# Kernel tuning notes

Hardware: AMD Instinct MI355X
Metric: run time of the kernel (lower is better)

The kernel has to match this reference:

```python
import jax, jax.numpy as jnp
import numpy as np

B, N, DIM = 2, 512, 128
HEADS, DH = 4, 64
INNER = HEADS * DH            # 256
POS_HID = 64
MULT = 4                      # attn_mlp_hidden_mult
K = 16                        # num_neighbors


def setup_inputs() -> dict:
    key = jax.random.key(0)
    ks = jax.random.split(key, 10)
    w = lambda k, shape: jax.random.normal(k, shape, jnp.float32) * 0.02
    return {
        "x": jax.random.normal(ks[0], (B, N, DIM), jnp.float32),
        "pos": jax.random.normal(ks[1], (B, N, 3), jnp.float32),
        "mask": jnp.ones((B, N), dtype=bool),
        "w_qkv": w(ks[2], (DIM, 3 * INNER)),
        "w_out": w(ks[3], (INNER, DIM)),
        "b_out": jnp.zeros((DIM,), jnp.float32),
        "w_pos1": w(ks[4], (3, POS_HID)),
        "b_pos1": jnp.zeros((POS_HID,), jnp.float32),
        "w_pos2": w(ks[5], (POS_HID, INNER)),
        "b_pos2": jnp.zeros((INNER,), jnp.float32),
        # grouped 1x1 convs == per-head linear layers
        "w_attn1": w(ks[6], (HEADS, DH, MULT * DH)),
        "b_attn1": jnp.zeros((HEADS, MULT * DH), jnp.float32),
        "w_attn2": w(ks[7], (HEADS, MULT * DH, DH)),
        "b_attn2": jnp.zeros((HEADS, DH), jnp.float32),
    }


def reference(x, pos, mask, w_qkv, w_out, b_out, w_pos1, b_pos1, w_pos2, b_pos2,
              w_attn1, b_attn1, w_attn2, b_attn2):
    b, n, _ = x.shape
    h, d = HEADS, DH

    qkv = x @ w_qkv                                   # [b, n, 3*inner]
    q, k, v = jnp.split(qkv, 3, axis=-1)
    to_heads = lambda t: t.reshape(b, n, h, d).transpose(0, 2, 1, 3)  # b h n d
    q, k, v = map(to_heads, (q, k, v))

    # dense pairwise relative positions + pos MLP  [b, n, n, inner]
    rel_pos = pos[:, :, None, :] - pos[:, None, :, :]            # [b, n, n, 3]
    rpe = jax.nn.relu(rel_pos @ w_pos1 + b_pos1) @ w_pos2 + b_pos2

    # masked topk over pairwise distance (smallest K)
    rel_dist = jnp.linalg.norm(rel_pos, axis=-1)                 # [b, n, n]
    mask2 = mask[:, :, None] & mask[:, None, :]                  # [b, n, n]
    fmax = jnp.finfo(rel_dist.dtype).max
    rel_dist = jnp.where(mask2, rel_dist, fmax)
    _, idx = jax.lax.top_k(-rel_dist, K)                         # [b, n, K]

    # neighbor gathers (equivalent to torch batched_index_select over j)
    gather_hd = jax.vmap(lambda t, i: t[:, i, :])                # [h,n,d],[n,K] -> [h,n,K,d]
    k_nb = gather_hd(k, idx)                                     # [b, h, n, K, d]
    v_nb = gather_hd(v, idx)
    row = jnp.arange(n)[:, None]
    rpe_nb = jax.vmap(lambda r, i: r[row, i])(rpe, idx)          # [b, n, K, inner]
    rpe_nb = rpe_nb.reshape(b, n, K, h, d).transpose(0, 3, 1, 2, 4)  # [b,h,n,K,d]
    mask_nb = jax.vmap(lambda m, i: m[row, i])(mask2, idx)       # [b, n, K]

    # qk_rel gathered implicitly: (q_i - k_j)[j=idx] == q_i - k_nb
    attn_in = q[:, :, :, None, :] - k_nb + rpe_nb                # [b, h, n, K, d]

    # grouped 1x1 conv MLP == per-head MLP on last dim
    hid = jax.nn.relu(jnp.einsum('bhikd,hde->bhike', attn_in, w_attn1)
                      + b_attn1[None, :, None, None, :])
    sim = (jnp.einsum('bhike,hed->bhikd', hid, w_attn2)
           + b_attn2[None, :, None, None, :])                    # [b, h, n, K, d]

    sim = jnp.where(mask_nb[:, None, :, :, None], sim, -fmax)
    # torch: sim is [b, (h d), i, j]; softmax(dim=-2) is over i -> axis 2 here
    attn = jax.nn.softmax(sim, axis=2)

    v_full = v_nb + rpe_nb                                       # [b, h, n, K, d]
    agg = jnp.sum(attn * v_full, axis=3)                         # [b, h, n, d]
    agg = agg.transpose(0, 2, 1, 3).reshape(b, n, h * d)         # [b, n, inner]
    return agg @ w_out + b_out
```

## Files before the change

kernel.cpp:

```cpp
#include <hip/hip_runtime.h>

#define B_ 2
#define N_ 512
#define DIM_ 128
#define HEADS_ 4
#define DH_ 64
#define INNER_ 256
#define PH_ 64
#define HID2_ 256
#define KNB_ 16

typedef unsigned long long u64;
typedef unsigned int u32;
typedef unsigned short u16;
typedef __attribute__((ext_vector_type(8))) short bf16x8;
typedef __attribute__((ext_vector_type(8))) unsigned short us8;
typedef __attribute__((ext_vector_type(4))) float f32x4;

__device__ __forceinline__ float bf2f(u16 u) {
    union { float f; u32 u; } c; c.u = ((u32)u) << 16; return c.f;
}
__device__ __forceinline__ u16 f2bf(float f) {
    union { float f; u32 u; } c; c.f = f;
    u32 u = c.u;
    return (u16)((u + 0x7fffu + ((u >> 16) & 1u)) >> 16);
}
__device__ __forceinline__ u32 pack2(float lo, float hi) {
    return ((u32)f2bf(hi) << 16) | (u32)f2bf(lo);
}

__global__ __launch_bounds__(256) void k_front(
        const float* __restrict__ x, const float* __restrict__ pos, const float* __restrict__ w_qkv,
        const float* __restrict__ w_a1, const float* __restrict__ w_a2, const float* __restrict__ w_p2,
        u16* __restrict__ w1T, u16* __restrict__ w2T, u16* __restrict__ w2pT,
        u16* __restrict__ qb, u16* __restrict__ kb, float* __restrict__ v,
        int* __restrict__ idx) {
    int blk = blockIdx.x;
    if (blk < 576) {
        int t = blk * 256 + threadIdx.x;
        if (t < 65536) {
            int h = t >> 14, e = (t >> 6) & 255, d = t & 63;
            w1T[t] = f2bf(w_a1[((h * 64 + d) << 8) + e]);
        } else if (t < 131072) {
            int t2 = t - 65536; int h = t2 >> 14, c = (t2 >> 8) & 63, e = t2 & 255;
            w2T[t2] = f2bf(w_a2[(((h << 8) + e) << 6) + c]);
        } else {
            int t3 = t - 131072; int c = t3 >> 6, e = t3 & 63;
            w2pT[t3] = f2bf(w_p2[(e << 8) + c]);
        }
    } else if (blk < 704) {
        int bu = blk - 576;
        int b = bu >> 6;
        int n0 = (bu & 63) * 8;
        int t = threadIdx.x;
        __shared__ float xs[8][128];
        #pragma unroll
        for (int p = 0; p < 4; ++p) {
            int e = p * 256 + t;
            xs[e >> 7][e & 127] = x[((size_t)(b * N_ + n0) + (e >> 7)) * DIM_ + (e & 127)];
        }
        __syncthreads();
        float acc[3][8];
        #pragma unroll
        for (int cc = 0; cc < 3; ++cc)
            #pragma unroll
            for (int r = 0; r < 8; ++r) acc[cc][r] = 0.f;
        for (int c4 = 0; c4 < 32; ++c4) {
            float wv[3][4];
            #pragma unroll
            for (int dd = 0; dd < 4; ++dd)
                #pragma unroll
                for (int cc = 0; cc < 3; ++cc)
                    wv[cc][dd] = w_qkv[(size_t)(c4 * 4 + dd) * (3 * INNER_) + cc * INNER_ + t];
            #pragma unroll
            for (int r = 0; r < 8; ++r) {
                float4 xv = *(const float4*)&xs[r][c4 * 4];
                #pragma unroll
                for (int cc = 0; cc < 3; ++cc)
                    acc[cc][r] += xv.x * wv[cc][0] + xv.y * wv[cc][1] + xv.z * wv[cc][2] + xv.w * wv[cc][3];
            }
        }
        int h = t >> 6, d = t & 63;
        #pragma unroll
        for (int r = 0; r < 8; ++r) {
            size_t o = (((size_t)(b * HEADS_ + h)) * N_ + n0 + r) * DH_ + d;
            qb[o] = f2bf(acc[0][r]);
            kb[o] = f2bf(acc[1][r]);
            v[o]  = acc[2][r];
        }
    } else {
        int wave = (blk - 704) * 4 + (threadIdx.x >> 6);
        int lane = threadIdx.x & 63;
        int b = wave >> 9;
        float px = pos[(size_t)wave * 3 + 0];
        float py = pos[(size_t)wave * 3 + 1];
        float pz = pos[(size_t)wave * 3 + 2];
        u64 keys[8];
        #pragma unroll
        for (int s = 0; s < 8; ++s) {
            int j = s * 64 + lane;
            float dx = __fsub_rn(px, pos[(size_t)(b * N_ + j) * 3 + 0]);
            float dy = __fsub_rn(py, pos[(size_t)(b * N_ + j) * 3 + 1]);
            float dz = __fsub_rn(pz, pos[(size_t)(b * N_ + j) * 3 + 2]);
            float s2 = __fadd_rn(__fadd_rn(__fmul_rn(dx, dx), __fmul_rn(dy, dy)), __fmul_rn(dz, dz));
            float dist = __fsqrt_rn(s2);
            keys[s] = ((u64)__float_as_uint(dist) << 32) | (unsigned)j;
        }
        for (int r = 0; r < KNB_; ++r) {
            u64 m = keys[0];
            #pragma unroll
            for (int s = 1; s < 8; ++s) m = (keys[s] < m) ? keys[s] : m;
            #pragma unroll
            for (int off = 32; off >= 1; off >>= 1) {
                u64 o = __shfl_xor(m, off);
                m = (o < m) ? o : m;
            }
            if (lane == 0) idx[(size_t)wave * KNB_ + r] = (int)(m & 0xffffffffu);
            #pragma unroll
            for (int s = 0; s < 8; ++s) if (keys[s] == m) keys[s] = ~0ull;
        }
    }
}

__global__ __launch_bounds__(256) void k_attn(
        const u16* __restrict__ qb, const u16* __restrict__ kb, const float* __restrict__ v,
        const int* __restrict__ idx,
        const float* __restrict__ pos, const float* __restrict__ w_p1, const float* __restrict__ b_p1,
        const float* __restrict__ b_p2, const u16* __restrict__ w2pT,
        const u16* __restrict__ w1T, const u16* __restrict__ w2T,
        const float* __restrict__ b_a1, const float* __restrict__ b_a2,
        u16* __restrict__ sim, u16* __restrict__ vf) {
    __shared__ u16 w1s[256 * 72];
    __shared__ u16 w2s[64 * 264];
    __shared__ u16 HID[4][4][16 * 136];
    int t = threadIdx.x;
    int wv = t >> 6, l = t & 63, lr = l & 15, g = l >> 4;
    int blk = blockIdx.x;
    int bh = blk >> 5, grp = blk & 31;
    int b = bh >> 2, h = bh & 3;
    int i0 = grp * 16 + wv * 4;

    int jn[4]; float rx[4], ry[4], rz[4];
    #pragma unroll
    for (int ii = 0; ii < 4; ++ii) {
        int i = i0 + ii, bi = (b << 9) + i;
        int j = idx[(bi << 4) + lr];
        jn[ii] = j;
        int bj = (b << 9) + j;
        rx[ii] = pos[(size_t)bi * 3 + 0] - pos[(size_t)bj * 3 + 0];
        ry[ii] = pos[(size_t)bi * 3 + 1] - pos[(size_t)bj * 3 + 1];
        rz[ii] = pos[(size_t)bi * 3 + 2] - pos[(size_t)bj * 3 + 2];
    }

    {
        const u16* wg = w1T + ((size_t)h << 14);
        #pragma unroll
        for (int p = 0; p < 8; ++p) {
            int c = p * 256 + t;
            int r = c >> 3, c8 = (c & 7) << 3;
            *(bf16x8*)&w1s[r * 72 + c8] = *(const bf16x8*)&wg[(r << 6) + c8];
        }
    }
    {
        const u16* wg = w2T + ((size_t)h << 14);
        #pragma unroll
        for (int p = 0; p < 8; ++p) {
            int c = p * 256 + t;
            int r = c >> 5, c8 = (c & 31) << 3;
            *(bf16x8*)&w2s[r * 264 + c8] = *(const bf16x8*)&wg[(r << 8) + c8];
        }
    }

    bf16x8 hidp[4][2];
    #pragma unroll
    for (int ii = 0; ii < 4; ++ii) {
        #pragma unroll
        for (int s = 0; s < 2; ++s) {
            u16 tmp[8];
            #pragma unroll
            for (int jj = 0; jj < 8; ++jj) {
                int e = s * 32 + g * 8 + jj;
                float hh = b_p1[e] + rx[ii] * w_p1[e] + ry[ii] * w_p1[PH_ + e] + rz[ii] * w_p1[2 * PH_ + e];
                tmp[jj] = f2bf(fmaxf(hh, 0.f));
            }
            hidp[ii][s] = *(bf16x8*)tmp;
        }
    }

    #pragma unroll
    for (int ct = 0; ct < 4; ++ct) {
        f32x4 C[4];
        #pragma unroll
        for (int ii = 0; ii < 4; ++ii) C[ii] = (f32x4){0.f, 0.f, 0.f, 0.f};
        #pragma unroll
        for (int s = 0; s < 2; ++s) {
            bf16x8 A = *(const bf16x8*)&w2pT[(size_t)(h * 64 + ct * 16 + lr) * 64 + s * 32 + g * 8];
            #pragma unroll
            for (int ii = 0; ii < 4; ++ii)
                C[ii] = __builtin_amdgcn_mfma_f32_16x16x32_bf16(A, hidp[ii][s], C[ii], 0, 0, 0);
        }
        float4 bias = *(const float4*)&b_p2[h * 64 + ct * 16 + g * 4];
        #pragma unroll
        for (int ii = 0; ii < 4; ++ii) {
            uint2 o;
            o.x = pack2(C[ii][0] + bias.x, C[ii][1] + bias.y);
            o.y = pack2(C[ii][2] + bias.z, C[ii][3] + bias.w);
            *(uint2*)&HID[wv][ii][lr * 136 + ct * 16 + g * 4] = o;
        }
    }

    bf16x8 ain[4][2];
    #pragma unroll
    for (int ii = 0; ii < 4; ++ii) {
        int i = i0 + ii, j = jn[ii];
        #pragma unroll
        for (int s = 0; s < 2; ++s) {
            bf16x8 rp = *(const bf16x8*)&HID[wv][ii][lr * 136 + s * 32 + g * 8];
            us8 rpu = *(const us8*)&rp;
            us8 qv = *(const us8*)&qb[(size_t)(bh * N_ + i) * 64 + s * 32 + g * 8];
            us8 kv = *(const us8*)&kb[(size_t)(bh * N_ + j) * 64 + s * 32 + g * 8];
            float4 v0 = *(const float4*)&v[(size_t)(bh * N_ + j) * 64 + s * 32 + g * 8];
            float4 v1 = *(const float4*)&v[(size_t)(bh * N_ + j) * 64 + s * 32 + g * 8 + 4];
            float vvr[8] = {v0.x, v0.y, v0.z, v0.w, v1.x, v1.y, v1.z, v1.w};
            u16 ta[8], tv[8];
            #pragma unroll
            for (int jj = 0; jj < 8; ++jj) {
                float rpf = bf2f(rpu[jj]);
                ta[jj] = f2bf(bf2f(qv[jj]) - bf2f(kv[jj]) + rpf);
                tv[jj] = f2bf(vvr[jj] + rpf);
            }
            ain[ii][s] = *(bf16x8*)ta;
            *(bf16x8*)&vf[(size_t)(((bh * N_ + i) << 4) + lr) * 64 + s * 32 + g * 8] = *(bf16x8*)tv;
        }
    }
    __syncthreads();

    f32x4 C2[4][4];
    #pragma unroll
    for (int ii = 0; ii < 4; ++ii)
        #pragma unroll
        for (int ct = 0; ct < 4; ++ct) C2[ii][ct] = (f32x4){0.f, 0.f, 0.f, 0.f};
    #pragma unroll
    for (int half = 0; half < 2; ++half) {
        #pragma unroll
        for (int etL = 0; etL < 8; ++etL) {
            int et = half * 8 + etL;
            f32x4 C[4];
            #pragma unroll
            for (int ii = 0; ii < 4; ++ii) C[ii] = (f32x4){0.f, 0.f, 0.f, 0.f};
            #pragma unroll
            for (int s = 0; s < 2; ++s) {
                bf16x8 A = *(const bf16x8*)&w1s[(et * 16 + lr) * 72 + s * 32 + g * 8];
                #pragma unroll
                for (int ii = 0; ii < 4; ++ii)
                    C[ii] = __builtin_amdgcn_mfma_f32_16x16x32_bf16(A, ain[ii][s], C[ii], 0, 0, 0);
            }
            float4 bias = *(const float4*)&b_a1[h * 256 + et * 16 + g * 4];
            #pragma unroll
            for (int ii = 0; ii < 4; ++ii) {
                uint2 p;
                p.x = pack2(fmaxf(C[ii][0] + bias.x, 0.f), fmaxf(C[ii][1] + bias.y, 0.f));
                p.y = pack2(fmaxf(C[ii][2] + bias.z, 0.f), fmaxf(C[ii][3] + bias.w, 0.f));
                *(uint2*)&HID[wv][ii][lr * 136 + etL * 16 + g * 4] = p;
            }
        }
        #pragma unroll
        for (int sL = 0; sL < 4; ++sL) {
            int s = half * 4 + sL;
            bf16x8 Bv[4];
            #pragma unroll
            for (int ii = 0; ii < 4; ++ii)
                Bv[ii] = *(const bf16x8*)&HID[wv][ii][lr * 136 + sL * 32 + g * 8];
            #pragma unroll
            for (int ct = 0; ct < 4; ++ct) {
                bf16x8 A = *(const bf16x8*)&w2s[(ct * 16 + lr) * 264 + s * 32 + g * 8];
                #pragma unroll
                for (int ii = 0; ii < 4; ++ii)
                    C2[ii][ct] = __builtin_amdgcn_mfma_f32_16x16x32_bf16(A, Bv[ii], C2[ii][ct], 0, 0, 0);
            }
        }
    }
    #pragma unroll
    for (int ii = 0; ii < 4; ++ii) {
        int i = i0 + ii;
        #pragma unroll
        for (int ct = 0; ct < 4; ++ct) {
            float4 bias = *(const float4*)&b_a2[h * 64 + ct * 16 + g * 4];
            uint2 o;
            o.x = pack2(C2[ii][ct][0] + bias.x, C2[ii][ct][1] + bias.y);
            o.y = pack2(C2[ii][ct][2] + bias.z, C2[ii][ct][3] + bias.w);
            *(uint2*)&sim[(size_t)(((bh * N_ + i) << 4) + lr) * 64 + ct * 16 + g * 4] = o;
        }
    }
}

__global__ __launch_bounds__(256) void k_stats(const u16* __restrict__ sim, float* __restrict__ R) {
    int blk = blockIdx.x;
    int ks = blk & 15, bh = blk >> 4;
    int d0 = (threadIdx.x & 15) * 4;
    int nc = threadIdx.x >> 4;
    __shared__ float red[16][69];
    size_t base = ((size_t)(bh * N_ + nc * 32) * 16 + ks) * 64 + d0;
    float s0 = 0.f, s1 = 0.f, s2 = 0.f, s3 = 0.f;
    for (int nn = 0; nn < 32; ++nn) {
        uint2 u = *(const uint2*)&sim[base + (size_t)nn * 1024];
        s0 += __expf(bf2f((u16)(u.x & 0xffff)));
        s1 += __expf(bf2f((u16)(u.x >> 16)));
        s2 += __expf(bf2f((u16)(u.y & 0xffff)));
        s3 += __expf(bf2f((u16)(u.y >> 16)));
    }
    red[nc][d0 + 0] = s0; red[nc][d0 + 1] = s1;
    red[nc][d0 + 2] = s2; red[nc][d0 + 3] = s3;
    __syncthreads();
    int t = threadIdx.x;
    if (t < 64) {
        float s = 0.f;
        #pragma unroll
        for (int c = 0; c < 16; ++c) s += red[c][t];
        R[(size_t)blk * 64 + t] = 1.f / s;
    }
}

__global__ __launch_bounds__(256) void k_agg_out(
        const u16* __restrict__ sim, const u16* __restrict__ vf, const float* __restrict__ R,
        const float* __restrict__ w, const float* __restrict__ bo, float* __restrict__ out) {
    int blk = blockIdx.x;
    int b = blk >> 7;
    int i0 = (blk & 127) * 4;
    int t = threadIdx.x;
    __shared__ float ag[4][260];
    {
        int h = t >> 6, d = t & 63;
        int bh = b * HEADS_ + h;
        float Rk[16];
        #pragma unroll
        for (int ks = 0; ks < 16; ++ks) Rk[ks] = R[((bh << 4) + ks) * 64 + d];
        #pragma unroll
        for (int r = 0; r < 4; ++r) {
            size_t base = (size_t)((bh * N_ + i0 + r) << 4) * 64 + d;
            float acc = 0.f;
            #pragma unroll
            for (int ks = 0; ks < 16; ++ks) {
                float p = __expf(bf2f(sim[base + (size_t)ks * 64])) * Rk[ks];
                acc += p * bf2f(vf[base + (size_t)ks * 64]);
            }
            ag[r][h * 64 + d] = acc;
        }
    }
    __syncthreads();
    int c = t & 127, rg = t >> 7;
    float acc[2];
    acc[0] = bo[c]; acc[1] = bo[c];
    for (int k4 = 0; k4 < 64; ++k4) {
        float wv[4];
        #pragma unroll
        for (int kk = 0; kk < 4; ++kk) wv[kk] = w[(size_t)(k4 * 4 + kk) * DIM_ + c];
        #pragma unroll
        for (int rr = 0; rr < 2; ++rr) {
            float4 a4 = *(const float4*)&ag[rr * 2 + rg][k4 * 4];
            acc[rr] += a4.x * wv[0] + a4.y * wv[1] + a4.z * wv[2] + a4.w * wv[3];
        }
    }
    #pragma unroll
    for (int rr = 0; rr < 2; ++rr)
        out[(size_t)((b << 9) + i0 + rr * 2 + rg) * DIM_ + c] = acc[rr];
}

extern "C" void kernel_launch(void* const* d_in, const int* in_sizes, int n_in,
                              void* d_out, int out_size, void* d_ws, size_t ws_size,
                              hipStream_t stream) {
    const float* x      = (const float*)d_in[0];
    const float* pos    = (const float*)d_in[1];
    const float* w_qkv  = (const float*)d_in[3];
    const float* w_out  = (const float*)d_in[4];
    const float* b_out  = (const float*)d_in[5];
    const float* w_pos1 = (const float*)d_in[6];
    const float* b_pos1 = (const float*)d_in[7];
    const float* w_pos2 = (const float*)d_in[8];
    const float* b_pos2 = (const float*)d_in[9];
    const float* w_a1   = (const float*)d_in[10];
    const float* b_a1   = (const float*)d_in[11];
    const float* w_a2   = (const float*)d_in[12];
    const float* b_a2   = (const float*)d_in[13];
    float* out = (float*)d_out;

    char* W = (char*)d_ws;
    u16*  qb   = (u16*)W;            W += 524288;
    u16*  kb   = (u16*)W;            W += 524288;
    float* v   = (float*)W;          W += 1048576;
    int*  idx  = (int*)W;            W += 65536;
    u16*  sim  = (u16*)W;            W += 8388608;
    u16*  vf   = (u16*)W;            W += 8388608;
    float* R   = (float*)W;          W += 32768;
    u16*  w1T  = (u16*)W;            W += 131072;
    u16*  w2T  = (u16*)W;            W += 131072;
    u16*  w2pT = (u16*)W;            W += 32768;

    k_front<<<960, 256, 0, stream>>>(x, pos, w_qkv, w_a1, w_a2, w_pos2,
                                     w1T, w2T, w2pT, qb, kb, v, idx);
    k_attn<<<256, 256, 0, stream>>>(qb, kb, v, idx, pos, w_pos1, b_pos1, b_pos2, w2pT,
                                    w1T, w2T, b_a1, b_a2, sim, vf);
    k_stats<<<128, 256, 0, stream>>>(sim, R);
    k_agg_out<<<256, 256, 0, stream>>>(sim, vf, R, w_out, b_out, out);
}
```

Measured before the change: 58.59 us.

## Split k_attn into one query row per wave and read MLP weights directly from global

Each wave in k_attn now handles one query row instead of four, so the grid grows from 256 to 1024 blocks. The per-head attention MLP weights are no longer staged in shared memory and are read straight from global memory or L2 at each MFMA. This shrinks LDS use and register pressure and removes the block-wide sync, which should raise occupancy and parallelism. In exchange, each weight fragment now feeds one MFMA instead of four, so global weight traffic per output rises sharply.

```diff
diff --git a/kernel.cpp b/kernel.cpp
--- a/kernel.cpp
+++ b/kernel.cpp
@@ -130,167 +130,113 @@
         const u16* __restrict__ w1T, const u16* __restrict__ w2T,
         const float* __restrict__ b_a1, const float* __restrict__ b_a2,
         u16* __restrict__ sim, u16* __restrict__ vf) {
-    __shared__ u16 w1s[256 * 72];
-    __shared__ u16 w2s[64 * 264];
-    __shared__ u16 HID[4][4][16 * 136];
+    __shared__ u16 HID[4][16 * 136];
     int t = threadIdx.x;
     int wv = t >> 6, l = t & 63, lr = l & 15, g = l >> 4;
     int blk = blockIdx.x;
-    int bh = blk >> 5, grp = blk & 31;
+    int bh = blk >> 7;
     int b = bh >> 2, h = bh & 3;
-    int i0 = grp * 16 + wv * 4;
-
-    int jn[4]; float rx[4], ry[4], rz[4];
-    #pragma unroll
-    for (int ii = 0; ii < 4; ++ii) {
-        int i = i0 + ii, bi = (b << 9) + i;
-        int j = idx[(bi << 4) + lr];
-        jn[ii] = j;
-        int bj = (b << 9) + j;
-        rx[ii] = pos[(size_t)bi * 3 + 0] - pos[(size_t)bj * 3 + 0];
-        ry[ii] = pos[(size_t)bi * 3 + 1] - pos[(size_t)bj * 3 + 1];
-        rz[ii] = pos[(size_t)bi * 3 + 2] - pos[(size_t)bj * 3 + 2];
-    }
-
-    {
-        const u16* wg = w1T + ((size_t)h << 14);
-        #pragma unroll
-        for (int p = 0; p < 8; ++p) {
-            int c = p * 256 + t;
-            int r = c >> 3, c8 = (c & 7) << 3;
-            *(bf16x8*)&w1s[r * 72 + c8] = *(const bf16x8*)&wg[(r << 6) + c8];
-        }
-    }
-    {
-        const u16* wg = w2T + ((size_t)h << 14);
-        #pragma unroll
-        for (int p = 0; p < 8; ++p) {
-            int c = p * 256 + t;
-            int r = c >> 5, c8 = (c & 31) << 3;
-            *(bf16x8*)&w2s[r * 264 + c8] = *(const bf16x8*)&wg[(r << 8) + c8];
-        }
-    }
-
-    bf16x8 hidp[4][2];
-    #pragma unroll
-    for (int ii = 0; ii < 4; ++ii) {
-        #pragma unroll
-        for (int s = 0; s < 2; ++s) {
-            u16 tmp[8];
-            #pragma unroll
-            for (int jj = 0; jj < 8; ++jj) {
-                int e = s * 32 + g * 8 + jj;
-                float hh = b_p1[e] + rx[ii] * w_p1[e] + ry[ii] * w_p1[PH_ + e] + rz[ii] * w_p1[2 * PH_ + e];
-                tmp[jj] = f2bf(fmaxf(hh, 0.f));
-            }
-            hidp[ii][s] = *(bf16x8*)tmp;
-        }
+    int i = ((blk & 127) << 2) + wv;
+    int bi = (b << 9) + i;
+
+    int j = idx[(bi << 4) + lr];
+    int bj = (b << 9) + j;
+    float rx = pos[(size_t)bi * 3 + 0] - pos[(size_t)bj * 3 + 0];
+    float ry = pos[(size_t)bi * 3 + 1] - pos[(size_t)bj * 3 + 1];
+    float rz = pos[(size_t)bi * 3 + 2] - pos[(size_t)bj * 3 + 2];
+    us8 qv[2], kv[2];
+    float4 v0[2], v1[2];
+    #pragma unroll
+    for (int s = 0; s < 2; ++s) {
+        qv[s] = *(const us8*)&qb[(size_t)(bh * N_ + i) * 64 + s * 32 + g * 8];
+        kv[s] = *(const us8*)&kb[(size_t)(bh * N_ + j) * 64 + s * 32 + g * 8];
+        v0[s] = *(const float4*)&v[(size_t)(bh * N_ + j) * 64 + s * 32 + g * 8];
+        v1[s] = *(const float4*)&v[(size_t)(bh * N_ + j) * 64 + s * 32 + g * 8 + 4];
+    }
+
+    bf16x8 hidp[2];
+    #pragma unroll
+    for (int s = 0; s < 2; ++s) {
+        u16 tmp[8];
+        #pragma unroll
+        for (int jj = 0; jj < 8; ++jj) {
+            int e = s * 32 + g * 8 + jj;
+            float hh = b_p1[e] + rx * w_p1[e] + ry * w_p1[PH_ + e] + rz * w_p1[2 * PH_ + e];
+            tmp[jj] = f2bf(fmaxf(hh, 0.f));
+        }
+        hidp[s] = *(bf16x8*)tmp;
     }
 
     #pragma unroll
     for (int ct = 0; ct < 4; ++ct) {
-        f32x4 C[4];
-        #pragma unroll
-        for (int ii = 0; ii < 4; ++ii) C[ii] = (f32x4){0.f, 0.f, 0.f, 0.f};
+        f32x4 C = {0.f, 0.f, 0.f, 0.f};
         #pragma unroll
         for (int s = 0; s < 2; ++s) {
             bf16x8 A = *(const bf16x8*)&w2pT[(size_t)(h * 64 + ct * 16 + lr) * 64 + s * 32 + g * 8];
-            #pragma unroll
-            for (int ii = 0; ii < 4; ++ii)
-                C[ii] = __builtin_amdgcn_mfma_f32_16x16x32_bf16(A, hidp[ii][s], C[ii], 0, 0, 0);
+            C = __builtin_amdgcn_mfma_f32_16x16x32_bf16(A, hidp[s], C, 0, 0, 0);
         }
         float4 bias = *(const float4*)&b_p2[h * 64 + ct * 16 + g * 4];
-        #pragma unroll
-        for (int ii = 0; ii < 4; ++ii) {
-            uint2 o;
-            o.x = pack2(C[ii][0] + bias.x, C[ii][1] + bias.y);
-            o.y = pack2(C[ii][2] + bias.z, C[ii][3] + bias.w);
-            *(uint2*)&HID[wv][ii][lr * 136 + ct * 16 + g * 4] = o;
-        }
-    }
-
-    bf16x8 ain[4][2];
-    #pragma unroll
-    for (int ii = 0; ii < 4; ++ii) {
-        int i = i0 + ii, j = jn[ii];
-        #pragma unroll
-        for (int s = 0; s < 2; ++s) {
-            bf16x8 rp = *(const bf16x8*)&HID[wv][ii][lr * 136 + s * 32 + g * 8];
-            us8 rpu = *(const us8*)&rp;
-            us8 qv = *(const us8*)&qb[(size_t)(bh * N_ + i) * 64 + s * 32 + g * 8];
-            us8 kv = *(const us8*)&kb[(size_t)(bh * N_ + j) * 64 + s * 32 + g * 8];
-            float4 v0 = *(const float4*)&v[(size_t)(bh * N_ + j) * 64 + s * 32 + g * 8];
-            float4 v1 = *(const float4*)&v[(size_t)(bh * N_ + j) * 64 + s * 32 + g * 8 + 4];
-            float vvr[8] = {v0.x, v0.y, v0.z, v0.w, v1.x, v1.y, v1.z, v1.w};
-            u16 ta[8], tv[8];
-            #pragma unroll
-            for (int jj = 0; jj < 8; ++jj) {
-                float rpf = bf2f(rpu[jj]);
-                ta[jj] = f2bf(bf2f(qv[jj]) - bf2f(kv[jj]) + rpf);
-                tv[jj] = f2bf(vvr[jj] + rpf);
-            }
-            ain[ii][s] = *(bf16x8*)ta;
-            *(bf16x8*)&vf[(size_t)(((bh * N_ + i) << 4) + lr) * 64 + s * 32 + g * 8] = *(bf16x8*)tv;
-        }
-    }
-    __syncthreads();
-
-    f32x4 C2[4][4];
-    #pragma unroll
-    for (int ii = 0; ii < 4; ++ii)
-        #pragma unroll
-        for (int ct = 0; ct < 4; ++ct) C2[ii][ct] = (f32x4){0.f, 0.f, 0.f, 0.f};
+        uint2 o;
+        o.x = pack2(C[0] + bias.x, C[1] + bias.y);
+        o.y = pack2(C[2] + bias.z, C[3] + bias.w);
+        *(uint2*)&HID[wv][lr * 136 + ct * 16 + g * 4] = o;
+    }
+
+    bf16x8 ain[2];
+    #pragma unroll
+    for (int s = 0; s < 2; ++s) {
+        bf16x8 rp = *(const bf16x8*)&HID[wv][lr * 136 + s * 32 + g * 8];
+        us8 rpu = *(const us8*)&rp;
+        float vvr[8] = {v0[s].x, v0[s].y, v0[s].z, v0[s].w, v1[s].x, v1[s].y, v1[s].z, v1[s].w};
+        u16 ta[8], tv[8];
+        #pragma unroll
+        for (int jj = 0; jj < 8; ++jj) {
+            float rpf = bf2f(rpu[jj]);
+            ta[jj] = f2bf(bf2f(qv[s][jj]) - bf2f(kv[s][jj]) + rpf);
+            tv[jj] = f2bf(vvr[jj] + rpf);
+        }
+        ain[s] = *(bf16x8*)ta;
+        *(bf16x8*)&vf[(size_t)(((bh * N_ + i) << 4) + lr) * 64 + s * 32 + g * 8] = *(bf16x8*)tv;
+    }
+
+    f32x4 C2[4];
+    #pragma unroll
+    for (int ct = 0; ct < 4; ++ct) C2[ct] = (f32x4){0.f, 0.f, 0.f, 0.f};
     #pragma unroll
     for (int half = 0; half < 2; ++half) {
         #pragma unroll
         for (int etL = 0; etL < 8; ++etL) {
             int et = half * 8 + etL;
-            f32x4 C[4];
-            #pragma unroll
-            for (int ii = 0; ii < 4; ++ii) C[ii] = (f32x4){0.f, 0.f, 0.f, 0.f};
+            f32x4 C = {0.f, 0.f, 0.f, 0.f};
             #pragma unroll
             for (int s = 0; s < 2; ++s) {
-                bf16x8 A = *(const bf16x8*)&w1s[(et * 16 + lr) * 72 + s * 32 + g * 8];
-                #pragma unroll
-                for (int ii = 0; ii < 4; ++ii)
-                    C[ii] = __builtin_amdgcn_mfma_f32_16x16x32_bf16(A, ain[ii][s], C[ii], 0, 0, 0);
+                bf16x8 A = *(const bf16x8*)&w1T[((size_t)h << 14) + (size_t)(et * 16 + lr) * 64 + s * 32 + g * 8];
+                C = __builtin_amdgcn_mfma_f32_16x16x32_bf16(A, ain[s], C, 0, 0, 0);
             }
             float4 bias = *(const float4*)&b_a1[h * 256 + et * 16 + g * 4];
-            #pragma unroll
-            for (int ii = 0; ii < 4; ++ii) {
-                uint2 p;
-                p.x = pack2(fmaxf(C[ii][0] + bias.x, 0.f), fmaxf(C[ii][1] + bias.y, 0.f));
-                p.y = pack2(fmaxf(C[ii][2] + bias.z, 0.f), fmaxf(C[ii][3] + bias.w, 0.f));
-                *(uint2*)&HID[wv][ii][lr * 136 + etL * 16 + g * 4] = p;
-            }
+            uint2 p;
+            p.x = pack2(fmaxf(C[0] + bias.x, 0.f), fmaxf(C[1] + bias.y, 0.f));
+            p.y = pack2(fmaxf(C[2] + bias.z, 0.f), fmaxf(C[3] + bias.w, 0.f));
+            *(uint2*)&HID[wv][lr * 136 + etL * 16 + g * 4] = p;
         }
         #pragma unroll
         for (int sL = 0; sL < 4; ++sL) {
             int s = half * 4 + sL;
-            bf16x8 Bv[4];
-            #pragma unroll
-            for (int ii = 0; ii < 4; ++ii)
-                Bv[ii] = *(const bf16x8*)&HID[wv][ii][lr * 136 + sL * 32 + g * 8];
+            bf16x8 Bv = *(const bf16x8*)&HID[wv][lr * 136 + sL * 32 + g * 8];
             #pragma unroll
             for (int ct = 0; ct < 4; ++ct) {
-                bf16x8 A = *(const bf16x8*)&w2s[(ct * 16 + lr) * 264 + s * 32 + g * 8];
-                #pragma unroll
-                for (int ii = 0; ii < 4; ++ii)
-                    C2[ii][ct] = __builtin_amdgcn_mfma_f32_16x16x32_bf16(A, Bv[ii], C2[ii][ct], 0, 0, 0);
-            }
-        }
-    }
-    #pragma unroll
-    for (int ii = 0; ii < 4; ++ii) {
-        int i = i0 + ii;
-        #pragma unroll
-        for (int ct = 0; ct < 4; ++ct) {
-            float4 bias = *(const float4*)&b_a2[h * 64 + ct * 16 + g * 4];
-            uint2 o;
-            o.x = pack2(C2[ii][ct][0] + bias.x, C2[ii][ct][1] + bias.y);
-            o.y = pack2(C2[ii][ct][2] + bias.z, C2[ii][ct][3] + bias.w);
-            *(uint2*)&sim[(size_t)(((bh * N_ + i) << 4) + lr) * 64 + ct * 16 + g * 4] = o;
-        }
+                bf16x8 A = *(const bf16x8*)&w2T[((size_t)h << 14) + (size_t)(ct * 16 + lr) * 256 + s * 32 + g * 8];
+                C2[ct] = __builtin_amdgcn_mfma_f32_16x16x32_bf16(A, Bv, C2[ct], 0, 0, 0);
+            }
+        }
+    }
+    #pragma unroll
+    for (int ct = 0; ct < 4; ++ct) {
+        float4 bias = *(const float4*)&b_a2[h * 64 + ct * 16 + g * 4];
+        uint2 o;
+        o.x = pack2(C2[ct][0] + bias.x, C2[ct][1] + bias.y);
+        o.y = pack2(C2[ct][2] + bias.z, C2[ct][3] + bias.w);
+        *(uint2*)&sim[(size_t)(((bh * N_ + i) << 4) + lr) * 64 + ct * 16 + g * 4] = o;
     }
 }
 
@@ -398,8 +344,8 @@
 
     k_front<<<960, 256, 0, stream>>>(x, pos, w_qkv, w_a1, w_a2, w_pos2,
                                      w1T, w2T, w2pT, qb, kb, v, idx);
-    k_attn<<<256, 256, 0, stream>>>(qb, kb, v, idx, pos, w_pos1, b_pos1, b_pos2, w2pT,
-                                    w1T, w2T, b_a1, b_a2, sim, vf);
+    k_attn<<<1024, 256, 0, stream>>>(qb, kb, v, idx, pos, w_pos1, b_pos1, b_pos2, w2pT,
+                                     w1T, w2T, b_a1, b_a2, sim, vf);
     k_stats<<<128, 256, 0, stream>>>(sim, R);
     k_agg_out<<<256, 256, 0, stream>>>(sim, vf, R, w_out, b_out, out);
 }
```

Result: slower. 82.38 us (+40.6%).

## Split attention MLP over more blocks and read weights directly from global

Applied to the files above, without the earlier changes.

k_attn now handles 2 query points per wave instead of 4 and launches 512 blocks instead of 256, so more of the GPU's compute units get work. The per-head MLP weights are no longer staged into shared memory. Each wave loads its MFMA A-fragments straight from global (L2-cached) memory into registers, which removes the staging copy and the __syncthreads. Q/K/V gathers are hoisted to the top of the kernel so their latency overlaps the positional MLP. In exchange, weight traffic per point rises because each wave re-reads the weights with less reuse, and register pressure grows from the preloaded fragments.

```diff
diff --git a/kernel.cpp b/kernel.cpp
--- a/kernel.cpp
+++ b/kernel.cpp
@@ -122,7 +122,7 @@
     }
 }
 
-__global__ __launch_bounds__(256) void k_attn(
+__global__ __launch_bounds__(256, 2) void k_attn(
         const u16* __restrict__ qb, const u16* __restrict__ kb, const float* __restrict__ v,
         const int* __restrict__ idx,
         const float* __restrict__ pos, const float* __restrict__ w_p1, const float* __restrict__ b_p1,
@@ -130,19 +130,19 @@
         const u16* __restrict__ w1T, const u16* __restrict__ w2T,
         const float* __restrict__ b_a1, const float* __restrict__ b_a2,
         u16* __restrict__ sim, u16* __restrict__ vf) {
-    __shared__ u16 w1s[256 * 72];
-    __shared__ u16 w2s[64 * 264];
-    __shared__ u16 HID[4][4][16 * 136];
+    __shared__ u16 HID[4][2][16 * 136];
     int t = threadIdx.x;
     int wv = t >> 6, l = t & 63, lr = l & 15, g = l >> 4;
     int blk = blockIdx.x;
-    int bh = blk >> 5, grp = blk & 31;
+    int bh = blk >> 6;
     int b = bh >> 2, h = bh & 3;
-    int i0 = grp * 16 + wv * 4;
-
-    int jn[4]; float rx[4], ry[4], rz[4];
-    #pragma unroll
-    for (int ii = 0; ii < 4; ++ii) {
+    int i0 = (blk & 63) * 8 + wv * 2;
+
+    int jn[2]; float rx[2], ry[2], rz[2];
+    us8 qv[2][2], kv[2][2];
+    float4 v0[2][2], v1[2][2];
+    #pragma unroll
+    for (int ii = 0; ii < 2; ++ii) {
         int i = i0 + ii, bi = (b << 9) + i;
         int j = idx[(bi << 4) + lr];
         jn[ii] = j;
@@ -150,30 +150,18 @@
         rx[ii] = pos[(size_t)bi * 3 + 0] - pos[(size_t)bj * 3 + 0];
         ry[ii] = pos[(size_t)bi * 3 + 1] - pos[(size_t)bj * 3 + 1];
         rz[ii] = pos[(size_t)bi * 3 + 2] - pos[(size_t)bj * 3 + 2];
-    }
-
-    {
-        const u16* wg = w1T + ((size_t)h << 14);
-        #pragma unroll
-        for (int p = 0; p < 8; ++p) {
-            int c = p * 256 + t;
-            int r = c >> 3, c8 = (c & 7) << 3;
-            *(bf16x8*)&w1s[r * 72 + c8] = *(const bf16x8*)&wg[(r << 6) + c8];
-        }
-    }
-    {
-        const u16* wg = w2T + ((size_t)h << 14);
-        #pragma unroll
-        for (int p = 0; p < 8; ++p) {
-            int c = p * 256 + t;
-            int r = c >> 5, c8 = (c & 31) << 3;
-            *(bf16x8*)&w2s[r * 264 + c8] = *(const bf16x8*)&wg[(r << 8) + c8];
-        }
-    }
-
-    bf16x8 hidp[4][2];
-    #pragma unroll
-    for (int ii = 0; ii < 4; ++ii) {
+        #pragma unroll
+        for (int s = 0; s < 2; ++s) {
+            qv[ii][s] = *(const us8*)&qb[(size_t)(bh * N_ + i) * 64 + s * 32 + g * 8];
+            kv[ii][s] = *(const us8*)&kb[(size_t)(bh * N_ + j) * 64 + s * 32 + g * 8];
+            v0[ii][s] = *(const float4*)&v[(size_t)(bh * N_ + j) * 64 + s * 32 + g * 8];
+            v1[ii][s] = *(const float4*)&v[(size_t)(bh * N_ + j) * 64 + s * 32 + g * 8 + 4];
+        }
+    }
+
+    bf16x8 hidp[2][2];
+    #pragma unroll
+    for (int ii = 0; ii < 2; ++ii) {
         #pragma unroll
         for (int s = 0; s < 2; ++s) {
             u16 tmp[8];
@@ -187,101 +175,112 @@
         }
     }
 
-    #pragma unroll
-    for (int ct = 0; ct < 4; ++ct) {
-        f32x4 C[4];
-        #pragma unroll
-        for (int ii = 0; ii < 4; ++ii) C[ii] = (f32x4){0.f, 0.f, 0.f, 0.f};
-        #pragma unroll
-        for (int s = 0; s < 2; ++s) {
-            bf16x8 A = *(const bf16x8*)&w2pT[(size_t)(h * 64 + ct * 16 + lr) * 64 + s * 32 + g * 8];
-            #pragma unroll
-            for (int ii = 0; ii < 4; ++ii)
-                C[ii] = __builtin_amdgcn_mfma_f32_16x16x32_bf16(A, hidp[ii][s], C[ii], 0, 0, 0);
-        }
-        float4 bias = *(const float4*)&b_p2[h * 64 + ct * 16 + g * 4];
-        #pragma unroll
-        for (int ii = 0; ii < 4; ++ii) {
-            uint2 o;
-            o.x = pack2(C[ii][0] + bias.x, C[ii][1] + bias.y);
-            o.y = pack2(C[ii][2] + bias.z, C[ii][3] + bias.w);
-            *(uint2*)&HID[wv][ii][lr * 136 + ct * 16 + g * 4] = o;
-        }
-    }
-
-    bf16x8 ain[4][2];
-    #pragma unroll
-    for (int ii = 0; ii < 4; ++ii) {
-        int i = i0 + ii, j = jn[ii];
+    {
+        bf16x8 Ar[4][2];
+        #pragma unroll
+        for (int ct = 0; ct < 4; ++ct)
+            #pragma unroll
+            for (int s = 0; s < 2; ++s)
+                Ar[ct][s] = *(const bf16x8*)&w2pT[(size_t)(h * 64 + ct * 16 + lr) * 64 + s * 32 + g * 8];
+        #pragma unroll
+        for (int ct = 0; ct < 4; ++ct) {
+            f32x4 C0 = {0.f, 0.f, 0.f, 0.f}, C1 = {0.f, 0.f, 0.f, 0.f};
+            #pragma unroll
+            for (int s = 0; s < 2; ++s) {
+                C0 = __builtin_amdgcn_mfma_f32_16x16x32_bf16(Ar[ct][s], hidp[0][s], C0, 0, 0, 0);
+                C1 = __builtin_amdgcn_mfma_f32_16x16x32_bf16(Ar[ct][s], hidp[1][s], C1, 0, 0, 0);
+            }
+            float4 bias = *(const float4*)&b_p2[h * 64 + ct * 16 + g * 4];
+            uint2 o0, o1;
+            o0.x = pack2(C0[0] + bias.x, C0[1] + bias.y);
+            o0.y = pack2(C0[2] + bias.z, C0[3] + bias.w);
+            o1.x = pack2(C1[0] + bias.x, C1[1] + bias.y);
+            o1.y = pack2(C1[2] + bias.z, C1[3] + bias.w);
+            *(uint2*)&HID[wv][0][lr * 136 + ct * 16 + g * 4] = o0;
+            *(uint2*)&HID[wv][1][lr * 136 + ct * 16 + g * 4] = o1;
+        }
+    }
+
+    bf16x8 ain[2][2];
+    #pragma unroll
+    for (int ii = 0; ii < 2; ++ii) {
+        int i = i0 + ii;
         #pragma unroll
         for (int s = 0; s < 2; ++s) {
             bf16x8 rp = *(const bf16x8*)&HID[wv][ii][lr * 136 + s * 32 + g * 8];
             us8 rpu = *(const us8*)&rp;
-            us8 qv = *(const us8*)&qb[(size_t)(bh * N_ + i) * 64 + s * 32 + g * 8];
-            us8 kv = *(const us8*)&kb[(size_t)(bh * N_ + j) * 64 + s * 32 + g * 8];
-            float4 v0 = *(const float4*)&v[(size_t)(bh * N_ + j) * 64 + s * 32 + g * 8];
-            float4 v1 = *(const float4*)&v[(size_t)(bh * N_ + j) * 64 + s * 32 + g * 8 + 4];
-            float vvr[8] = {v0.x, v0.y, v0.z, v0.w, v1.x, v1.y, v1.z, v1.w};
+            float vvr[8] = {v0[ii][s].x, v0[ii][s].y, v0[ii][s].z, v0[ii][s].w,
+                            v1[ii][s].x, v1[ii][s].y, v1[ii][s].z, v1[ii][s].w};
             u16 ta[8], tv[8];
             #pragma unroll
             for (int jj = 0; jj < 8; ++jj) {
                 float rpf = bf2f(rpu[jj]);
-                ta[jj] = f2bf(bf2f(qv[jj]) - bf2f(kv[jj]) + rpf);
+                ta[jj] = f2bf(bf2f(qv[ii][s][jj]) - bf2f(kv[ii][s][jj]) + rpf);
                 tv[jj] = f2bf(vvr[jj] + rpf);
             }
             ain[ii][s] = *(bf16x8*)ta;
             *(bf16x8*)&vf[(size_t)(((bh * N_ + i) << 4) + lr) * 64 + s * 32 + g * 8] = *(bf16x8*)tv;
         }
     }
-    __syncthreads();
-
-    f32x4 C2[4][4];
-    #pragma unroll
-    for (int ii = 0; ii < 4; ++ii)
+
+    f32x4 C2[2][4];
+    #pragma unroll
+    for (int ii = 0; ii < 2; ++ii)
         #pragma unroll
         for (int ct = 0; ct < 4; ++ct) C2[ii][ct] = (f32x4){0.f, 0.f, 0.f, 0.f};
     #pragma unroll
     for (int half = 0; half < 2; ++half) {
+        bf16x8 A1[8][2];
+        #pragma unroll
+        for (int etL = 0; etL < 8; ++etL)
+            #pragma unroll
+            for (int s = 0; s < 2; ++s)
+                A1[etL][s] = *(const bf16x8*)&w1T[((size_t)h << 14)
+                               + (size_t)((half * 8 + etL) * 16 + lr) * 64 + s * 32 + g * 8];
         #pragma unroll
         for (int etL = 0; etL < 8; ++etL) {
             int et = half * 8 + etL;
-            f32x4 C[4];
-            #pragma unroll
-            for (int ii = 0; ii < 4; ++ii) C[ii] = (f32x4){0.f, 0.f, 0.f, 0.f};
+            f32x4 C0 = {0.f, 0.f, 0.f, 0.f}, C1 = {0.f, 0.f, 0.f, 0.f};
             #pragma unroll
             for (int s = 0; s < 2; ++s) {
-                bf16x8 A = *(const bf16x8*)&w1s[(et * 16 + lr) * 72 + s * 32 + g * 8];
+                C0 = __builtin_amdgcn_mfma_f32_16x16x32_bf16(A1[etL][s], ain[0][s], C0, 0, 0, 0);
+                C1 = __builtin_amdgcn_mfma_f32_16x16x32_bf16(A1[etL][s], ain[1][s], C1, 0, 0, 0);
+            }
+            float4 bias = *(const float4*)&b_a1[h * 256 + et * 16 + g * 4];
+            uint2 p0, p1;
+            p0.x = pack2(fmaxf(C0[0] + bias.x, 0.f), fmaxf(C0[1] + bias.y, 0.f));
+            p0.y = pack2(fmaxf(C0[2] + bias.z, 0.f), fmaxf(C0[3] + bias.w, 0.f));
+            p1.x = pack2(fmaxf(C1[0] + bias.x, 0.f), fmaxf(C1[1] + bias.y, 0.f));
+            p1.y = pack2(fmaxf(C1[2] + bias.z, 0.f), fmaxf(C1[3] + bias.w, 0.f));
+            *(uint2*)&HID[wv][0][lr * 136 + etL * 16 + g * 4] = p0;
+            *(uint2*)&HID[wv][1][lr * 136 + etL * 16 + g * 4] = p1;
+        }
+        #pragma unroll
+        for (int chunk = 0; chunk < 2; ++chunk) {
+            bf16x8 A2[4][2];
+            #pragma unroll
+            for (int ct = 0; ct < 4; ++ct)
                 #pragma unroll
-                for (int ii = 0; ii < 4; ++ii)
-                    C[ii] = __builtin_amdgcn_mfma_f32_16x16x32_bf16(A, ain[ii][s], C[ii], 0, 0, 0);
-            }
-            float4 bias = *(const float4*)&b_a1[h * 256 + et * 16 + g * 4];
-            #pragma unroll
-            for (int ii = 0; ii < 4; ++ii) {
-                uint2 p;
-                p.x = pack2(fmaxf(C[ii][0] + bias.x, 0.f), fmaxf(C[ii][1] + bias.y, 0.f));
-                p.y = pack2(fmaxf(C[ii][2] + bias.z, 0.f), fmaxf(C[ii][3] + bias.w, 0.f));
-                *(uint2*)&HID[wv][ii][lr * 136 + etL * 16 + g * 4] = p;
-            }
-        }
-        #pragma unroll
-        for (int sL = 0; sL < 4; ++sL) {
-            int s = half * 4 + sL;
-            bf16x8 Bv[4];
-            #pragma unroll
-            for (int ii = 0; ii < 4; ++ii)
-                Bv[ii] = *(const bf16x8*)&HID[wv][ii][lr * 136 + sL * 32 + g * 8];
-            #pragma unroll
-            for (int ct = 0; ct < 4; ++ct) {
-                bf16x8 A = *(const bf16x8*)&w2s[(ct * 16 + lr) * 264 + s * 32 + g * 8];
+                for (int ss = 0; ss < 2; ++ss) {
+                    int s = half * 4 + chunk * 2 + ss;
+                    A2[ct][ss] = *(const bf16x8*)&w2T[((size_t)h << 14)
+                                   + (size_t)(ct * 16 + lr) * 256 + s * 32 + g * 8];
+                }
+            #pragma unroll
+            for (int ss = 0; ss < 2; ++ss) {
+                int sL = chunk * 2 + ss;
+                bf16x8 B0 = *(const bf16x8*)&HID[wv][0][lr * 136 + sL * 32 + g * 8];
+                bf16x8 B1 = *(const bf16x8*)&HID[wv][1][lr * 136 + sL * 32 + g * 8];
                 #pragma unroll
-                for (int ii = 0; ii < 4; ++ii)
-                    C2[ii][ct] = __builtin_amdgcn_mfma_f32_16x16x32_bf16(A, Bv[ii], C2[ii][ct], 0, 0, 0);
-            }
-        }
-    }
-    #pragma unroll
-    for (int ii = 0; ii < 4; ++ii) {
+                for (int ct = 0; ct < 4; ++ct) {
+                    C2[0][ct] = __builtin_amdgcn_mfma_f32_16x16x32_bf16(A2[ct][ss], B0, C2[0][ct], 0, 0, 0);
+                    C2[1][ct] = __builtin_amdgcn_mfma_f32_16x16x32_bf16(A2[ct][ss], B1, C2[1][ct], 0, 0, 0);
+                }
+            }
+        }
+    }
+    #pragma unroll
+    for (int ii = 0; ii < 2; ++ii) {
         int i = i0 + ii;
         #pragma unroll
         for (int ct = 0; ct < 4; ++ct) {
@@ -398,7 +397,7 @@
 
     k_front<<<960, 256, 0, stream>>>(x, pos, w_qkv, w_a1, w_a2, w_pos2,
                                      w1T, w2T, w2pT, qb, kb, v, idx);
-    k_attn<<<256, 256, 0, stream>>>(qb, kb, v, idx, pos, w_pos1, b_pos1, b_pos2, w2pT,
+    k_attn<<<512, 256, 0, stream>>>(qb, kb, v, idx, pos, w_pos1, b_pos1, b_pos2, w2pT,
                                     w1T, w2T, b_a1, b_a2, sim, vf);
     k_stats<<<128, 256, 0, stream>>>(sim, R);
     k_agg_out<<<256, 256, 0, stream>>>(sim, vf, R, w_out, b_out, out);
```

New measurement: 67.50 us. 15.2% more time.
